# Optimization experiments

Hardware: AMD Instinct MI355X
Metric: run time of the kernel (lower is better)

Reference implementation:

```python
import jax, jax.numpy as jnp
import numpy as np

N_ENT = 50000
N_REL = 16
N_EDGE = 1000000
D = 64


def setup_inputs() -> dict:
    key = jax.random.key(0)
    ks = jax.random.split(key, 20)
    inp = {
        'ent_embed': jax.random.normal(ks[0], (N_ENT, D), jnp.float32) * 0.1,
        'rel_embed': jax.random.normal(ks[1], (N_REL, D), jnp.float32) * 0.1,
        'W_R': jax.random.normal(ks[2], (N_REL, D, D), jnp.float32) * 0.1,
        'W1_0': jax.random.normal(ks[3], (64, 64), jnp.float32) * 0.1,
        'b1_0': jax.random.normal(ks[4], (64,), jnp.float32) * 0.1,
        'W2_0': jax.random.normal(ks[5], (64, 64), jnp.float32) * 0.1,
        'b2_0': jax.random.normal(ks[6], (64,), jnp.float32) * 0.1,
        'W1_1': jax.random.normal(ks[7], (64, 32), jnp.float32) * 0.1,
        'b1_1': jax.random.normal(ks[8], (32,), jnp.float32) * 0.1,
        'W2_1': jax.random.normal(ks[9], (64, 32), jnp.float32) * 0.1,
        'b2_1': jax.random.normal(ks[10], (32,), jnp.float32) * 0.1,
        'W1_2': jax.random.normal(ks[11], (32, 16), jnp.float32) * 0.1,
        'b1_2': jax.random.normal(ks[12], (16,), jnp.float32) * 0.1,
        'W2_2': jax.random.normal(ks[13], (32, 16), jnp.float32) * 0.1,
        'b2_2': jax.random.normal(ks[14], (16,), jnp.float32) * 0.1,
        'src': jax.random.randint(ks[15], (N_EDGE,), 0, N_ENT, jnp.int32),
        'dst': jax.random.randint(ks[16], (N_EDGE,), 0, N_ENT, jnp.int32),
        'etype': jax.random.randint(ks[17], (N_EDGE,), 0, N_REL, jnp.int32),
    }
    return inp


def _l2_normalize(x, eps=1e-12):
    # matches torch F.normalize(p=2, dim=1)
    n = jnp.sqrt(jnp.sum(x * x, axis=1, keepdims=True))
    return x / jnp.maximum(n, eps)


def _kgat_forward(ent_embed, rel_embed, W_R, layer_params, src, dst, etype):
    N = ent_embed.shape[0]
    # --- compute_attention: per-relation TransR projection of all entities ---
    # equivalent to per-edge ent[src] @ W_R[type] without materializing [E, D, D]
    proj = jnp.einsum('nd,rde->rne', ent_embed, W_R)          # [R, N, D]
    r_mul_t = proj[etype, src]                                # [E, D] (tail = src)
    r_mul_h = proj[etype, dst]                                # [E, D] (head = dst)
    att = jnp.sum(r_mul_t * jnp.tanh(r_mul_h + rel_embed[etype]), axis=-1)  # [E]
    # edge softmax grouped by destination node
    m = jax.ops.segment_max(att, dst, num_segments=N)         # [N]
    e = jnp.exp(att - m[dst])
    s = jax.ops.segment_sum(e, dst, num_segments=N)           # [N]
    a = e / s[dst]                                            # [E]

    # --- cf_embedding: bi-interaction aggregator layers ---
    h = ent_embed
    all_embed = [h]
    for (W1, b1, W2, b2) in layer_params:
        msg = a[:, None] * h[src]                             # [E, d_in]
        N_h = jax.ops.segment_sum(msg, dst, num_segments=N)   # [N, d_in]
        out = (jax.nn.leaky_relu((h + N_h) @ W1 + b1, 0.01)
               + jax.nn.leaky_relu((h * N_h) @ W2 + b2, 0.01))
        h = out
        all_embed.append(_l2_normalize(out))
    return jnp.concatenate(all_embed, axis=1)                 # [N, 64+64+32+16=176]


def reference(ent_embed, rel_embed, W_R,
              W1_0, b1_0, W2_0, b2_0,
              W1_1, b1_1, W2_1, b2_1,
              W1_2, b1_2, W2_2, b2_2,
              src, dst, etype):
    layer_params = [(W1_0, b1_0, W2_0, b2_0),
                    (W1_1, b1_1, W2_1, b2_1),
                    (W1_2, b1_2, W2_2, b2_2)]
    return _kgat_forward(ent_embed, rel_embed, W_R, layer_params, src, dst, etype)
```

## Files before the change

### kernel.cpp

```cpp
#include <hip/hip_runtime.h>
#include <hip/hip_bf16.h>
#include <cmath>

#define N_ENT  50000
#define N_RELS 16
#define N_EDGE 1000000
#define DIM    64
#define OUT_STRIDE 176

typedef float f32x4 __attribute__((ext_vector_type(4)));
typedef short s16x8 __attribute__((ext_vector_type(8)));

__device__ inline void bf16x8_unpack(uint4 u, float* f) {
    f[0] = __uint_as_float((u.x & 0xffffu) << 16);
    f[1] = __uint_as_float(u.x & 0xffff0000u);
    f[2] = __uint_as_float((u.y & 0xffffu) << 16);
    f[3] = __uint_as_float(u.y & 0xffff0000u);
    f[4] = __uint_as_float((u.z & 0xffffu) << 16);
    f[5] = __uint_as_float(u.z & 0xffff0000u);
    f[6] = __uint_as_float((u.w & 0xffffu) << 16);
    f[7] = __uint_as_float(u.w & 0xffff0000u);
}

__device__ inline ushort f2bf(float x) {
    __hip_bfloat16 b = __float2bfloat16(x);
    return *(ushort*)&b;
}

__device__ inline uint cvt_pk_bf16(float lo, float hi) {
    uint r;
    asm("v_cvt_pk_bf16_f32 %0, %1, %2" : "=v"(r) : "v"(lo), "v"(hi));
    return r;
}

__device__ __host__ inline int pcol(int p) {
    int qp = (p >> 3) & 7;
    int k  = p & 7;
    return 16 * (k >> 1) + 2 * qp + (k & 1);
}

__global__ __launch_bounds__(256) void prep_convert_kernel(
        const float* __restrict__ ent,
        ushort* __restrict__ ent_pi,
        float* __restrict__ out) {
    int i = blockIdx.x * blockDim.x + threadIdx.x;
    if (i < N_ENT * DIM) {
        float v = ent[i];
        ushort b = f2bf(v);
        int n = i >> 6, c = i & 63;
        int pos = ((c & 15) >> 1) * 8 + ((c >> 4) << 1) + (c & 1);
        ent_pi[(size_t)n * 64 + pos] = b;
        out[(size_t)n * OUT_STRIDE + c] = v;
    }
}

__global__ __launch_bounds__(256) void scan1_kernel(
        const int* __restrict__ counts, int* __restrict__ excl,
        int* __restrict__ bsum, int n) {
    __shared__ int sh[256];
    int t = threadIdx.x;
    int i = blockIdx.x * 256 + t;
    int c = (i < n) ? counts[i] : 0;
    sh[t] = c;
    __syncthreads();
    for (int off = 1; off < 256; off <<= 1) {
        int v = (t >= off) ? sh[t - off] : 0;
        __syncthreads();
        sh[t] += v;
        __syncthreads();
    }
    if (i < n) excl[i] = sh[t] - c;
    if (t == 255) bsum[blockIdx.x] = sh[255];
}

__global__ __launch_bounds__(256) void scan2_kernel(
        const int* __restrict__ bsum, int* __restrict__ boff,
        int* __restrict__ row_ptr, int nb, int n) {
    __shared__ int sh[256];
    int t = threadIdx.x;
    int v = (t < nb) ? bsum[t] : 0;
    sh[t] = v;
    __syncthreads();
    for (int off = 1; off < 256; off <<= 1) {
        int x = (t >= off) ? sh[t - off] : 0;
        __syncthreads();
        sh[t] += x;
        __syncthreads();
    }
    if (t < nb) boff[t] = sh[t] - v;
    if (t == nb - 1) row_ptr[n] = sh[t];
}

__global__ __launch_bounds__(256) void scan3_pos_kernel(
        const int* __restrict__ excl, const int* __restrict__ boff,
        int* __restrict__ row_ptr,
        const int* __restrict__ src, const int* __restrict__ dst,
        const int* __restrict__ etype, const int* __restrict__ off,
        unsigned long long* __restrict__ einfo) {
    int i = blockIdx.x * blockDim.x + threadIdx.x;
    if (i < N_ENT) row_ptr[i] = excl[i] + boff[i >> 8];
    if (i < N_EDGE) {
        int d = dst[i];
        int pos = excl[d] + boff[d >> 8] + off[i];
        unsigned long long info =
              (unsigned long long)(unsigned)src[i]
            | ((unsigned long long)(unsigned)d << 16)
            | ((unsigned long long)(unsigned)etype[i] << 32);
        einfo[pos] = info;
    }
}

__device__ __forceinline__ void gz_body(
        int r, int wid, int nw, int lane,
        const ushort* __restrict__ ent_pi,
        const float*  __restrict__ W_R,
        const float*  __restrict__ rel,
        ushort* __restrict__ Z,
        float* __restrict__ myLds) {
    int m = lane & 15;
    int q = lane >> 4;

    const float* Wr = W_R + (size_t)r * DIM * DIM;
    s16x8 b1[4][2], b2[4][2];
#pragma unroll
    for (int c = 0; c < 4; ++c)
#pragma unroll
        for (int ch = 0; ch < 2; ++ch)
#pragma unroll
            for (int j = 0; j < 8; ++j) {
                b1[c][ch][j] = (short)f2bf(Wr[pcol(ch * 32 + q * 8 + j) * DIM + c * 16 + m]);
                b2[c][ch][j] = (short)f2bf(Wr[(c * 16 + m) * DIM + ch * 32 + q * 8 + j]);
            }
    float relv[4];
#pragma unroll
    for (int c = 0; c < 4; ++c) relv[c] = rel[r * DIM + c * 16 + m];

    int par = m & 1;
    const int ntiles = N_ENT / 16;

    for (int t = wid; t < ntiles; t += nw) {
        int row0 = t * 16;
        const s16x8* arow = (const s16x8*)(ent_pi + (size_t)(row0 + m) * DIM);
        s16x8 a0 = arow[q];
        s16x8 a1 = arow[4 + q];
        f32x4 acc[4];
#pragma unroll
        for (int c = 0; c < 4; ++c) acc[c] = (f32x4){0.f, 0.f, 0.f, 0.f};
#pragma unroll
        for (int c = 0; c < 4; ++c) {
            acc[c] = __builtin_amdgcn_mfma_f32_16x16x32_bf16(a0, b1[c][0], acc[c], 0, 0, 0);
            acc[c] = __builtin_amdgcn_mfma_f32_16x16x32_bf16(a1, b1[c][1], acc[c], 0, 0, 0);
        }
#pragma unroll
        for (int c = 0; c < 4; ++c)
#pragma unroll
            for (int i = 0; i < 4; ++i) {
                float x = acc[c][i] + relv[c];
                float e2 = __expf(2.f * x);
                float g = 1.f - 2.f * __builtin_amdgcn_rcpf(e2 + 1.f);
                myLds[(q * 4 + i) * 68 + c * 16 + m] = g;
            }
        union { uint u[4]; s16x8 v; } a2u[2];
#pragma unroll
        for (int ch = 0; ch < 2; ++ch) {
            const f32x4* gp = (const f32x4*)(myLds + m * 68 + ch * 32 + q * 8);
            f32x4 g0 = gp[0];
            f32x4 g1 = gp[1];
            a2u[ch].u[0] = cvt_pk_bf16(g0[0], g0[1]);
            a2u[ch].u[1] = cvt_pk_bf16(g0[2], g0[3]);
            a2u[ch].u[2] = cvt_pk_bf16(g1[0], g1[1]);
            a2u[ch].u[3] = cvt_pk_bf16(g1[2], g1[3]);
        }

        f32x4 zacc[4];
#pragma unroll
        for (int c = 0; c < 4; ++c) zacc[c] = (f32x4){0.f, 0.f, 0.f, 0.f};
#pragma unroll
        for (int c = 0; c < 4; ++c) {
            zacc[c] = __builtin_amdgcn_mfma_f32_16x16x32_bf16(a2u[0].v, b2[c][0], zacc[c], 0, 0, 0);
            zacc[c] = __builtin_amdgcn_mfma_f32_16x16x32_bf16(a2u[1].v, b2[c][1], zacc[c], 0, 0, 0);
        }

        int rowA = row0 + 4 * q + (par ? 2 : 0);
        ushort* zb = Z + ((size_t)r * N_ENT + rowA) * 64 + (m >> 1) * 8;
#pragma unroll
        for (int rep = 0; rep < 2; ++rep) {
            uint4 Wv;
#pragma unroll
            for (int c = 0; c < 4; ++c) {
                float send = par ? zacc[c][rep] : zacc[c][2 + rep];
                float own  = par ? zacc[c][2 + rep] : zacc[c][rep];
                float oth  = __shfl_xor(send, 1, 64);
                float lo = par ? oth : own;
                float hi = par ? own : oth;
                ((uint*)&Wv)[c] = cvt_pk_bf16(lo, hi);
            }
            *(uint4*)(zb + rep * 64) = Wv;
        }
    }
}

#define HIST_LANES 32768

__global__ __launch_bounds__(512, 4) void gz_hist_kernel(
        const ushort* __restrict__ ent_pi,
        const float*  __restrict__ W_R,
        const float*  __restrict__ rel,
        ushort* __restrict__ Z,
        const int* __restrict__ dst,
        int* __restrict__ counts,
        int* __restrict__ off) {
    __shared__ __align__(16) float lds[7][16 * 68 + 16];
    int lane = threadIdx.x & 63;
    int wv   = threadIdx.x >> 6;

    if (wv == 7) {
        int lane_gid = blockIdx.x * 64 + lane;
#pragma unroll
        for (int half = 0; half < 2; ++half) {
            int d[16]; bool v[16]; int o[16];
#pragma unroll
            for (int k = 0; k < 16; ++k) {
                int i = lane_gid + (half * 16 + k) * HIST_LANES;
                v[k] = (i < N_EDGE);
                d[k] = v[k] ? dst[i] : 0;
            }
#pragma unroll
            for (int k = 0; k < 16; ++k)
                if (v[k]) o[k] = atomicAdd(&counts[d[k]], 1);
#pragma unroll
            for (int k = 0; k < 16; ++k)
                if (v[k]) off[lane_gid + (half * 16 + k) * HIST_LANES] = o[k];
        }
        return;
    }

    int r   = blockIdx.x >> 5;
    int xb  = blockIdx.x & 31;
    int wid = xb * 7 + wv;
    gz_body(r, wid, 224, lane, ent_pi, W_R, rel, Z, lds[wv]);
}

__global__ __launch_bounds__(256) void att_dot_kernel(
        const ushort* __restrict__ ent_pi,
        const ushort* __restrict__ Z,
        const unsigned long long* __restrict__ einfo,
        uint2* __restrict__ es_csr,
        int n_edge) {
    int tid  = blockIdx.x * blockDim.x + threadIdx.x;
    int lane = threadIdx.x & 63;
    int sub  = lane >> 3;
    int q    = lane & 7;
    int base = (tid >> 6) * 32;
    if (base >= n_edge) return;

    int e[4];
    unsigned long long inf[4];
#pragma unroll
    for (int k = 0; k < 4; ++k) {
        e[k] = base + k * 8 + sub;
        inf[k] = einfo[e[k]];
    }

    int s[4], p_r[4], p_d[4];
#pragma unroll
    for (int k = 0; k < 4; ++k) {
        s[k]   = (int)(inf[k] & 0xffffu);
        p_d[k] = (int)((inf[k] >> 16) & 0xffffu);
        p_r[k] = (int)((inf[k] >> 32) & 0xfu);
    }

    uint4 uz[4], ue[4];
#pragma unroll
    for (int k = 0; k < 4; ++k) {
        uz[k] = *(const uint4*)(Z + ((size_t)p_r[k] * N_ENT + p_d[k]) * DIM + q * 8);
        ue[k] = *(const uint4*)(ent_pi + (size_t)s[k] * DIM + q * 8);
    }

    float pr[4];
#pragma unroll
    for (int k = 0; k < 4; ++k) {
        float zv[8], ev[8];
        bf16x8_unpack(uz[k], zv);
        bf16x8_unpack(ue[k], ev);
        float p = 0.f;
#pragma unroll
        for (int j = 0; j < 8; ++j) p = fmaf(ev[j], zv[j], p);
        pr[k] = p;
    }
#pragma unroll
    for (int k = 0; k < 4; ++k) {
        pr[k] += __shfl_xor(pr[k], 1, 64);
        pr[k] += __shfl_xor(pr[k], 2, 64);
        pr[k] += __shfl_xor(pr[k], 4, 64);
    }

    if (q == 0) {
#pragma unroll
        for (int k = 0; k < 4; ++k)
            es_csr[e[k]] = make_uint2(__float_as_uint(pr[k]), (unsigned)s[k]);
    }
}

__global__ __launch_bounds__(256) void stats_kernel(
        const int* __restrict__ row_ptr, const uint2* __restrict__ es_csr,
        float2* __restrict__ stats, int n_node) {
    int wid  = (blockIdx.x * blockDim.x + threadIdx.x) >> 6;
    int lane = threadIdx.x & 63;
    if (wid >= n_node) return;
    int start = row_ptr[wid], end = row_ptr[wid + 1];

    float m = -INFINITY;
    for (int i = start + lane; i < end; i += 64)
        m = fmaxf(m, __uint_as_float(es_csr[i].x));
#pragma unroll
    for (int off = 32; off > 0; off >>= 1)
        m = fmaxf(m, __shfl_xor(m, off, 64));

    float ssum = 0.f;
    for (int i = start + lane; i < end; i += 64)
        ssum += __expf(__uint_as_float(es_csr[i].x) - m);
#pragma unroll
    for (int off = 32; off > 0; off >>= 1)
        ssum += __shfl_xor(ssum, off, 64);

    if (lane == 0)
        stats[wid] = make_float2(m, (end > start) ? (1.0f / ssum) : 0.f);
}

__global__ __launch_bounds__(256) void agg64_kernel(
        const ushort* __restrict__ tab,
        const uint2* __restrict__ es_csr,
        const int* __restrict__ row_ptr,
        const float2* __restrict__ stats,
        float* __restrict__ N_h, int n_node) {
    int wid  = (blockIdx.x * blockDim.x + threadIdx.x) >> 6;
    int lane = threadIdx.x & 63;
    if (wid >= n_node) return;
    int q   = lane & 7;
    int sub = lane >> 3;

    int start = row_ptr[wid], end = row_ptr[wid + 1];
    float2 st = stats[wid];
    float mx = st.x, inv = st.y;
    float acc[8];
#pragma unroll
    for (int j = 0; j < 8; ++j) acc[j] = 0.f;

    for (int p = start + sub; p < end; p += 8) {
        uint2 es = es_csr[p];
        float av = __expf(__uint_as_float(es.x) - mx);
        int   si = (int)es.y;
        uint4 u  = *(const uint4*)(tab + (size_t)si * 64 + q * 8);
        float g[8];
        bf16x8_unpack(u, g);
#pragma unroll
        for (int j = 0; j < 8; ++j) acc[j] = fmaf(av, g[j], acc[j]);
    }
#pragma unroll
    for (int mask = 8; mask < 64; mask <<= 1)
#pragma unroll
        for (int j = 0; j < 8; ++j)
            acc[j] += __shfl_xor(acc[j], mask, 64);

    if (sub == 0) {
        float* dstp = N_h + (size_t)wid * 64 + q * 8;
        *(float4*)(dstp)     = (float4){acc[0] * inv, acc[1] * inv, acc[2] * inv, acc[3] * inv};
        *(float4*)(dstp + 4) = (float4){acc[4] * inv, acc[5] * inv, acc[6] * inv, acc[7] * inv};
    }
}

__global__ __launch_bounds__(256) void agg32_kernel(
        const ushort* __restrict__ tab,
        const uint2* __restrict__ es_csr,
        const int* __restrict__ row_ptr,
        const float2* __restrict__ stats,
        float* __restrict__ N_h, int n_node) {
    int wid  = (blockIdx.x * blockDim.x + threadIdx.x) >> 6;
    int lane = threadIdx.x & 63;
    if (wid >= n_node) return;
    int q   = lane & 3;
    int sub = lane >> 2;

    int start = row_ptr[wid], end = row_ptr[wid + 1];
    float2 st = stats[wid];
    float mx = st.x, inv = st.y;
    float acc[8];
#pragma unroll
    for (int j = 0; j < 8; ++j) acc[j] = 0.f;

    for (int p = start + sub; p < end; p += 16) {
        uint2 es = es_csr[p];
        float av = __expf(__uint_as_float(es.x) - mx);
        int   si = (int)es.y;
        uint4 u  = *(const uint4*)(tab + (size_t)si * 32 + q * 8);
        float g[8];
        bf16x8_unpack(u, g);
#pragma unroll
        for (int j = 0; j < 8; ++j) acc[j] = fmaf(av, g[j], acc[j]);
    }
#pragma unroll
    for (int mask = 4; mask < 64; mask <<= 1)
#pragma unroll
        for (int j = 0; j < 8; ++j)
            acc[j] += __shfl_xor(acc[j], mask, 64);

    if (sub == 0) {
        float* dstp = N_h + (size_t)wid * 32 + q * 8;
        *(float4*)(dstp)     = (float4){acc[0] * inv, acc[1] * inv, acc[2] * inv, acc[3] * inv};
        *(float4*)(dstp + 4) = (float4){acc[4] * inv, acc[5] * inv, acc[6] * inv, acc[7] * inv};
    }
}

template <int D_IN, int D_OUT, bool PERM>
__global__ __launch_bounds__(256) void mlp_mfma_kernel(
        const ushort* __restrict__ h,
        const float* __restrict__ N_h,
        const float* __restrict__ W1, const float* __restrict__ b1,
        const float* __restrict__ W2, const float* __restrict__ b2,
        ushort* __restrict__ ho,
        float* __restrict__ out_buf, int out_col) {
    constexpr int CH = D_IN / 32;
    constexpr int CT = D_OUT / 16;

    int lane = threadIdx.x & 63;
    int m    = lane & 15;
    int q    = lane >> 4;
    int wid  = blockIdx.x * (blockDim.x >> 6) + (threadIdx.x >> 6);
    int nw   = gridDim.x * (blockDim.x >> 6);

    s16x8 bu[CT][CH], bv[CT][CH];
#pragma unroll
    for (int c = 0; c < CT; ++c)
#pragma unroll
        for (int ch = 0; ch < CH; ++ch)
#pragma unroll
            for (int j = 0; j < 8; ++j) {
                int p = ch * 32 + q * 8 + j;
                int k = PERM ? pcol(p) : p;
                bu[c][ch][j] = (short)f2bf(W1[k * D_OUT + c * 16 + m]);
                bv[c][ch][j] = (short)f2bf(W2[k * D_OUT + c * 16 + m]);
            }

    const int ntiles = N_ENT / 16;
    for (int t = wid; t < ntiles; t += nw) {
        int row0 = t * 16;
        s16x8 au[CH], av[CH];
#pragma unroll
        for (int ch = 0; ch < CH; ++ch) {
            uint4 hu = *(const uint4*)(h + (size_t)(row0 + m) * D_IN + ch * 32 + q * 8);
            float hv8[8];
            bf16x8_unpack(hu, hv8);
            const float4* np = (const float4*)(N_h + (size_t)(row0 + m) * D_IN + ch * 32 + q * 8);
            float4 na = np[0], nb = np[1];
            float nv[8] = {na.x, na.y, na.z, na.w, nb.x, nb.y, nb.z, nb.w};
#pragma unroll
            for (int j = 0; j < 8; ++j) {
                au[ch][j] = (short)f2bf(hv8[j] + nv[j]);
                av[ch][j] = (short)f2bf(hv8[j] * nv[j]);
            }
        }

        f32x4 accu[CT], accv[CT];
#pragma unroll
        for (int c = 0; c < CT; ++c) {
            accu[c] = (f32x4){0.f, 0.f, 0.f, 0.f};
            accv[c] = (f32x4){0.f, 0.f, 0.f, 0.f};
        }
#pragma unroll
        for (int c = 0; c < CT; ++c)
#pragma unroll
            for (int ch = 0; ch < CH; ++ch) {
                accu[c] = __builtin_amdgcn_mfma_f32_16x16x32_bf16(au[ch], bu[c][ch], accu[c], 0, 0, 0);
                accv[c] = __builtin_amdgcn_mfma_f32_16x16x32_bf16(av[ch], bv[c][ch], accv[c], 0, 0, 0);
            }

        float res[CT][4];
        float sq[4] = {0.f, 0.f, 0.f, 0.f};
#pragma unroll
        for (int c = 0; c < CT; ++c) {
            float bb1 = b1[c * 16 + m];
            float bb2 = b2[c * 16 + m];
#pragma unroll
            for (int i = 0; i < 4; ++i) {
                float o1 = accu[c][i] + bb1;
                float o2 = accv[c][i] + bb2;
                float r1 = (o1 >= 0.f) ? o1 : 0.01f * o1;
                float r2 = (o2 >= 0.f) ? o2 : 0.01f * o2;
                float rr = r1 + r2;
                res[c][i] = rr;
                sq[i] = fmaf(rr, rr, sq[i]);
            }
        }
#pragma unroll
        for (int mask = 1; mask < 16; mask <<= 1)
#pragma unroll
            for (int i = 0; i < 4; ++i)
                sq[i] += __shfl_xor(sq[i], mask, 64);

#pragma unroll
        for (int i = 0; i < 4; ++i) {
            int row = row0 + q * 4 + i;
            float inv = 1.f / fmaxf(sqrtf(sq[i]), 1e-12f);
#pragma unroll
            for (int c = 0; c < CT; ++c) {
                int col = c * 16 + m;
                out_buf[(size_t)row * OUT_STRIDE + out_col + col] = res[c][i] * inv;
                if (ho) ho[(size_t)row * D_OUT + col] = f2bf(res[c][i]);
            }
        }
    }
}

extern "C" void kernel_launch(void* const* d_in, const int* in_sizes, int n_in,
                              void* d_out, int out_size, void* d_ws, size_t ws_size,
                              hipStream_t stream) {
    const float* ent  = (const float*)d_in[0];
    const float* rel  = (const float*)d_in[1];
    const float* W_R  = (const float*)d_in[2];
    const float* W1_0 = (const float*)d_in[3];
    const float* b1_0 = (const float*)d_in[4];
    const float* W2_0 = (const float*)d_in[5];
    const float* b2_0 = (const float*)d_in[6];
    const float* W1_1 = (const float*)d_in[7];
    const float* b1_1 = (const float*)d_in[8];
    const float* W2_1 = (const float*)d_in[9];
    const float* b2_1 = (const float*)d_in[10];
    const float* W1_2 = (const float*)d_in[11];
    const float* b1_2 = (const float*)d_in[12];
    const float* W2_2 = (const float*)d_in[13];
    const float* b2_2 = (const float*)d_in[14];
    const int*   src   = (const int*)d_in[15];
    const int*   dst   = (const int*)d_in[16];
    const int*   etype = (const int*)d_in[17];
    float* out = (float*)d_out;

    char* w = (char*)d_ws;
    uint2*  es_csr  = (uint2*)w;  w += (size_t)N_EDGE * 8;
    int*    counts  = (int*)w;    w += (size_t)(N_ENT + 64) * 4;
    int*    row_ptr = (int*)w;    w += (size_t)(N_ENT + 64) * 4;
    float2* stats   = (float2*)w; w += (size_t)(N_ENT + 64) * 8;
    int*    excl    = (int*)w;    w += (size_t)(N_ENT + 64) * 4;
    int*    bsum    = (int*)w;    w += 256 * 4;
    int*    boff    = (int*)w;    w += 256 * 4;
    ushort* ent_pi  = (ushort*)w; w += (size_t)N_ENT * 64 * 2;
    ushort* h1      = (ushort*)w; w += (size_t)N_ENT * 64 * 2;
    ushort* h2      = (ushort*)w; w += (size_t)N_ENT * 32 * 2;
    float*  N_h     = (float*)w;  w += (size_t)N_ENT * 64 * 4;
    ushort* Z       = (ushort*)w;
    (void)ws_size;

    int* off = (int*)es_csr;
    unsigned long long* einfo = (unsigned long long*)N_h;

    hipMemsetAsync(counts, 0, (size_t)N_ENT * 4, stream);

    const int nb = (N_ENT + 255) / 256;

    prep_convert_kernel<<<(N_ENT * DIM + 255) / 256, 256, 0, stream>>>(
        ent, ent_pi, out);

    gz_hist_kernel<<<512, 512, 0, stream>>>(
        ent_pi, W_R, rel, Z, dst, counts, off);

    scan1_kernel<<<nb, 256, 0, stream>>>(counts, excl, bsum, N_ENT);
    scan2_kernel<<<1, 256, 0, stream>>>(bsum, boff, row_ptr, nb, N_ENT);
    scan3_pos_kernel<<<(N_EDGE + 255) / 256, 256, 0, stream>>>(
        excl, boff, row_ptr, src, dst, etype, off, einfo);

    att_dot_kernel<<<((N_EDGE + 31) / 32 * 64 + 255) / 256, 256, 0, stream>>>(
        ent_pi, Z, einfo, es_csr, N_EDGE);

    stats_kernel<<<(N_ENT + 3) / 4, 256, 0, stream>>>(row_ptr, es_csr, stats, N_ENT);

    const int aggGrid = (N_ENT + 3) / 4;
    const int mlpGrid = 782;

    agg64_kernel<<<aggGrid, 256, 0, stream>>>(ent_pi, es_csr, row_ptr, stats, N_h, N_ENT);
    mlp_mfma_kernel<64, 64, true><<<mlpGrid, 256, 0, stream>>>(
        ent_pi, N_h, W1_0, b1_0, W2_0, b2_0, h1, out, 64);

    agg64_kernel<<<aggGrid, 256, 0, stream>>>(h1, es_csr, row_ptr, stats, N_h, N_ENT);
    mlp_mfma_kernel<64, 32, false><<<mlpGrid, 256, 0, stream>>>(
        h1, N_h, W1_1, b1_1, W2_1, b2_1, h2, out, 128);

    agg32_kernel<<<aggGrid, 256, 0, stream>>>(h2, es_csr, row_ptr, stats, N_h, N_ENT);
    mlp_mfma_kernel<32, 16, false><<<mlpGrid, 256, 0, stream>>>(
        h2, N_h, W1_2, b1_2, W2_2, b2_2, nullptr, out, 160);
}
```

Measured before the change: 372.3 us.

## Fuse softmax stats into first aggregation and reshape gz/hist block layout

```diff
diff --git a/kernel.cpp b/kernel.cpp
--- a/kernel.cpp
+++ b/kernel.cpp
@@ -200,9 +200,9 @@
     }
 }
 
-#define HIST_LANES 32768
-
-__global__ __launch_bounds__(512, 4) void gz_hist_kernel(
+#define HIST_LANES 131072
+
+__global__ __launch_bounds__(256, 4) void gz_hist_kernel(
         const ushort* __restrict__ ent_pi,
         const float*  __restrict__ W_R,
         const float*  __restrict__ rel,
@@ -210,35 +210,32 @@
         const int* __restrict__ dst,
         int* __restrict__ counts,
         int* __restrict__ off) {
-    __shared__ __align__(16) float lds[7][16 * 68 + 16];
+    __shared__ __align__(16) float lds[3][16 * 68 + 16];
     int lane = threadIdx.x & 63;
     int wv   = threadIdx.x >> 6;
 
-    if (wv == 7) {
+    if (wv == 3) {
         int lane_gid = blockIdx.x * 64 + lane;
-#pragma unroll
-        for (int half = 0; half < 2; ++half) {
-            int d[16]; bool v[16]; int o[16];
-#pragma unroll
-            for (int k = 0; k < 16; ++k) {
-                int i = lane_gid + (half * 16 + k) * HIST_LANES;
-                v[k] = (i < N_EDGE);
-                d[k] = v[k] ? dst[i] : 0;
-            }
-#pragma unroll
-            for (int k = 0; k < 16; ++k)
-                if (v[k]) o[k] = atomicAdd(&counts[d[k]], 1);
-#pragma unroll
-            for (int k = 0; k < 16; ++k)
-                if (v[k]) off[lane_gid + (half * 16 + k) * HIST_LANES] = o[k];
-        }
+        int d[8]; bool v[8]; int o[8];
+#pragma unroll
+        for (int k = 0; k < 8; ++k) {
+            int i = lane_gid + k * HIST_LANES;
+            v[k] = (i < N_EDGE);
+            d[k] = v[k] ? dst[i] : 0;
+        }
+#pragma unroll
+        for (int k = 0; k < 8; ++k)
+            if (v[k]) o[k] = atomicAdd(&counts[d[k]], 1);
+#pragma unroll
+        for (int k = 0; k < 8; ++k)
+            if (v[k]) off[lane_gid + k * HIST_LANES] = o[k];
         return;
     }
 
-    int r   = blockIdx.x >> 5;
-    int xb  = blockIdx.x & 31;
-    int wid = xb * 7 + wv;
-    gz_body(r, wid, 224, lane, ent_pi, W_R, rel, Z, lds[wv]);
+    int r   = blockIdx.x >> 7;
+    int xb  = blockIdx.x & 127;
+    int wid = xb * 3 + wv;
+    gz_body(r, wid, 384, lane, ent_pi, W_R, rel, Z, lds[wv]);
 }
 
 __global__ __launch_bounds__(256) void att_dot_kernel(
@@ -302,30 +299,60 @@
     }
 }
 
-__global__ __launch_bounds__(256) void stats_kernel(
-        const int* __restrict__ row_ptr, const uint2* __restrict__ es_csr,
-        float2* __restrict__ stats, int n_node) {
+__global__ __launch_bounds__(256) void agg64s_kernel(
+        const ushort* __restrict__ tab,
+        const uint2* __restrict__ es_csr,
+        const int* __restrict__ row_ptr,
+        float2* __restrict__ stats,
+        float* __restrict__ N_h, int n_node) {
     int wid  = (blockIdx.x * blockDim.x + threadIdx.x) >> 6;
     int lane = threadIdx.x & 63;
     if (wid >= n_node) return;
+    int q   = lane & 7;
+    int sub = lane >> 3;
+
     int start = row_ptr[wid], end = row_ptr[wid + 1];
 
-    float m = -INFINITY;
+    float mx = -INFINITY;
     for (int i = start + lane; i < end; i += 64)
-        m = fmaxf(m, __uint_as_float(es_csr[i].x));
-#pragma unroll
-    for (int off = 32; off > 0; off >>= 1)
-        m = fmaxf(m, __shfl_xor(m, off, 64));
-
+        mx = fmaxf(mx, __uint_as_float(es_csr[i].x));
+#pragma unroll
+    for (int o = 32; o > 0; o >>= 1)
+        mx = fmaxf(mx, __shfl_xor(mx, o, 64));
     float ssum = 0.f;
     for (int i = start + lane; i < end; i += 64)
-        ssum += __expf(__uint_as_float(es_csr[i].x) - m);
-#pragma unroll
-    for (int off = 32; off > 0; off >>= 1)
-        ssum += __shfl_xor(ssum, off, 64);
-
-    if (lane == 0)
-        stats[wid] = make_float2(m, (end > start) ? (1.0f / ssum) : 0.f);
+        ssum += __expf(__uint_as_float(es_csr[i].x) - mx);
+#pragma unroll
+    for (int o = 32; o > 0; o >>= 1)
+        ssum += __shfl_xor(ssum, o, 64);
+    float inv = (end > start) ? (1.0f / ssum) : 0.f;
+    if (lane == 0) stats[wid] = make_float2(mx, inv);
+
+    float acc[8];
+#pragma unroll
+    for (int j = 0; j < 8; ++j) acc[j] = 0.f;
+
+    for (int p = start + sub; p < end; p += 8) {
+        uint2 es = es_csr[p];
+        float av = __expf(__uint_as_float(es.x) - mx);
+        int   si = (int)es.y;
+        uint4 u  = *(const uint4*)(tab + (size_t)si * 64 + q * 8);
+        float g[8];
+        bf16x8_unpack(u, g);
+#pragma unroll
+        for (int j = 0; j < 8; ++j) acc[j] = fmaf(av, g[j], acc[j]);
+    }
+#pragma unroll
+    for (int mask = 8; mask < 64; mask <<= 1)
+#pragma unroll
+        for (int j = 0; j < 8; ++j)
+            acc[j] += __shfl_xor(acc[j], mask, 64);
+
+    if (sub == 0) {
+        float* dstp = N_h + (size_t)wid * 64 + q * 8;
+        *(float4*)(dstp)     = (float4){acc[0] * inv, acc[1] * inv, acc[2] * inv, acc[3] * inv};
+        *(float4*)(dstp + 4) = (float4){acc[4] * inv, acc[5] * inv, acc[6] * inv, acc[7] * inv};
+    }
 }
 
 __global__ __launch_bounds__(256) void agg64_kernel(
@@ -560,7 +587,7 @@
     prep_convert_kernel<<<(N_ENT * DIM + 255) / 256, 256, 0, stream>>>(
         ent, ent_pi, out);
 
-    gz_hist_kernel<<<512, 512, 0, stream>>>(
+    gz_hist_kernel<<<2048, 256, 0, stream>>>(
         ent_pi, W_R, rel, Z, dst, counts, off);
 
     scan1_kernel<<<nb, 256, 0, stream>>>(counts, excl, bsum, N_ENT);
@@ -571,12 +598,10 @@
     att_dot_kernel<<<((N_EDGE + 31) / 32 * 64 + 255) / 256, 256, 0, stream>>>(
         ent_pi, Z, einfo, es_csr, N_EDGE);
 
-    stats_kernel<<<(N_ENT + 3) / 4, 256, 0, stream>>>(row_ptr, es_csr, stats, N_ENT);
-
     const int aggGrid = (N_ENT + 3) / 4;
     const int mlpGrid = 782;
 
-    agg64_kernel<<<aggGrid, 256, 0, stream>>>(ent_pi, es_csr, row_ptr, stats, N_h, N_ENT);
+    agg64s_kernel<<<aggGrid, 256, 0, stream>>>(ent_pi, es_csr, row_ptr, stats, N_h, N_ENT);
     mlp_mfma_kernel<64, 64, true><<<mlpGrid, 256, 0, stream>>>(
         ent_pi, N_h, W1_0, b1_0, W2_0, b2_0, h1, out, 64);
 
```

After: 363.4 us. 1.02x faster.
